# Kernel optimization log

Measured on AMD Instinct MI355X. Metric: run time of the kernel, lower is better.

Reference implementation:

```python
import jax, jax.numpy as jnp
import numpy as np

APPERTURE = 256
LN_EPS = 1e-3  # keras LayerNormalization default


def _layernorm(x, gamma, beta):
    mu = jnp.mean(x, axis=-1, keepdims=True)
    var = jnp.mean(jnp.square(x - mu), axis=-1, keepdims=True)
    return (x - mu) * jax.lax.rsqrt(var + LN_EPS) * gamma + beta


def setup_inputs() -> dict:
    key = jax.random.key(0)
    ks = jax.random.split(key, 8)
    n, d = 4096, 1024
    s = 0.02
    return {
        "x": jax.random.normal(ks[0], (1, n, d), jnp.float32),
        "wk": s * jax.random.normal(ks[1], (d, d), jnp.float32),
        "wq": s * jax.random.normal(ks[2], (d, d), jnp.float32),
        "wv": s * jax.random.normal(ks[3], (d, d), jnp.float32),
        "wo": s * jax.random.normal(ks[4], (d, d), jnp.float32),
        "wka": s * jax.random.normal(ks[5], (d, d), jnp.float32),
        "bka": jnp.zeros((d,), jnp.float32),
        "wkd": s * jax.random.normal(ks[6], (d, 1), jnp.float32),
        "bkd": jnp.zeros((1,), jnp.float32),
        "g_y": jnp.ones((d,), jnp.float32),
        "b_y": jnp.zeros((d,), jnp.float32),
        "g_ka": jnp.ones((d,), jnp.float32),
        "b_ka": jnp.zeros((d,), jnp.float32),
    }


def reference(x, wk, wq, wv, wo, wka, bka, wkd, bkd, g_y, b_y, g_ka, b_ka):
    m = x.shape[2]
    xf = x.reshape(-1, m)            # (n, m); seqlen == max_seqlen so no pad/trunc
    n = xf.shape[0]
    K = xf @ wk                      # (n, d)
    Q = (xf @ wq) * 0.06             # (n, d)
    V = xf @ wv                      # (n, d)
    logits = Q @ K.T                 # (n, n)
    # banded (apperture) mask: entries with |i-j| > apperture -> -inf
    idx = jnp.arange(n)
    band = jnp.abs(idx[:, None] - idx[None, :]) <= APPERTURE
    logits = jnp.where(band, logits, -jnp.inf)
    weights = jax.nn.softmax(logits, axis=0)   # softmax over queries (axis 0), as in original
    # y = transpose(V^T @ W) = W^T @ V
    y = weights.T @ V                # (n, d)
    y = y @ wo + xf                  # output_linear (no bias) + residual
    y = _layernorm(y, g_y, b_y)
    y = jax.nn.relu(y @ wka + bka)
    y = _layernorm(y, g_ka, b_ka)
    y = jax.nn.sigmoid(y @ wkd + bkd)  # (n, 1)
    return y.reshape(1, -1)            # (1, n)
```

## Files before the change

kernel.cpp:

```cpp
#include <hip/hip_runtime.h>
#include <hip/hip_bf16.h>
#include <math.h>

typedef __hip_bfloat16 bf16;
typedef __attribute__((ext_vector_type(8))) short bf16x8;
typedef __attribute__((ext_vector_type(4))) float f32x4;

#define NROW 4096
#define DIM  1024
#define APP  256
#define KQS  2048
#define WIN  640
#define VTPW 4608

__device__ __forceinline__ unsigned short f2bu(float f) {
    bf16 h = __float2bfloat16(f);
    return *reinterpret_cast<unsigned short*>(&h);
}
__device__ __forceinline__ float bu2f(unsigned short u) {
    bf16 h; *reinterpret_cast<unsigned short*>(&h) = u;
    return __bfloat162float(h);
}
__device__ __forceinline__ unsigned pk2(float a, float b) {
    return (unsigned)f2bu(a) | ((unsigned)f2bu(b) << 16);
}
__device__ __forceinline__ void gload_lds16(const void* g, void* l) {
    __builtin_amdgcn_global_load_lds(
        (const __attribute__((address_space(1))) unsigned int*)g,
        (__attribute__((address_space(3))) unsigned int*)l, 16, 0, 0);
}

__global__ __launch_bounds__(256) void zero_pads_kernel(bf16* __restrict__ Vtp) {
    int idx = blockIdx.x * 256 + threadIdx.x;
    int row = idx >> 7;
    int c4  = idx & 127;
    int col = (c4 < 64) ? (c4 * 4) : (4352 + (c4 - 64) * 4);
    *(uint2*)(Vtp + (size_t)row * VTPW + col) = (uint2){0u, 0u};
}

__global__ __launch_bounds__(256) void cast_x_kernel(const float* __restrict__ x,
                                                     bf16* __restrict__ xb) {
    int idx = blockIdx.x * 256 + threadIdx.x;
    float4 v = ((const float4*)x)[idx];
    uint2 o; o.x = pk2(v.x, v.y); o.y = pk2(v.z, v.w);
    ((uint2*)xb)[idx] = o;
}

struct WPtrs { const float* s[5]; bf16* d[5]; };
__global__ __launch_bounds__(256) void tcast_kernel(WPtrs p) {
    __shared__ float T[64][65];
    const float* in = p.s[blockIdx.z];
    bf16* out = p.d[blockIdx.z];
    const int t = threadIdx.x;
    const int r0 = blockIdx.x * 64, c0 = blockIdx.y * 64;
    if (blockIdx.z == 4) {
        #pragma unroll
        for (int c = 0; c < 4; ++c) {
            int row = (t >> 4) + c * 16, col = (t & 15) * 4;
            float4 v = *(const float4*)(in + (size_t)(r0 + row) * 1024 + c0 + col);
            uint2 o; o.x = pk2(v.x, v.y); o.y = pk2(v.z, v.w);
            *(uint2*)(out + (size_t)(r0 + row) * 1024 + c0 + col) = o;
        }
        return;
    }
    #pragma unroll
    for (int c = 0; c < 4; ++c) {
        int row = (t >> 4) + c * 16, col = (t & 15) * 4;
        float4 v = *(const float4*)(in + (size_t)(r0 + row) * 1024 + c0 + col);
        T[row][col] = v.x; T[row][col + 1] = v.y; T[row][col + 2] = v.z; T[row][col + 3] = v.w;
    }
    __syncthreads();
    #pragma unroll
    for (int c = 0; c < 4; ++c) {
        int orow = (t >> 4) + c * 16, ocol = (t & 15) * 4;
        uint2 o;
        o.x = pk2(T[ocol][orow], T[ocol + 1][orow]);
        o.y = pk2(T[ocol + 2][orow], T[ocol + 3][orow]);
        *(uint2*)(out + (size_t)(c0 + orow) * 1024 + r0 + ocol) = o;
    }
}

template <int BM, int BN>
__global__ __launch_bounds__(256) void gemm_bt(
    const bf16* __restrict__ A, int lda, const bf16* __restrict__ Bt, int ldb,
    bf16* __restrict__ C, int ldc, int K,
    float alpha, const float* __restrict__ bias, int relu, int pv)
{
    constexpr int WM = BM / 2, WN = BN / 2, AI = WM / 16, BJ = WN / 16;
    __shared__ bf16 As[BM * 64];
    __shared__ bf16 Bs[BN * 64];
    const int t = threadIdx.x, l = t & 63, w = t >> 6;
    const int wr = w >> 1, wc = w & 1;
    const int jl = l & 15, g = l >> 4;
    const int m0 = blockIdx.y * BM, n0 = blockIdx.x * BN;
    const bf16* Btb = pv ? (Bt + (size_t)(m0 >> 7) * 128) : Bt;

    f32x4 acc[AI][BJ];
    #pragma unroll
    for (int i = 0; i < AI; ++i)
        #pragma unroll
        for (int j = 0; j < BJ; ++j) acc[i][j] = (f32x4){0.f, 0.f, 0.f, 0.f};

    for (int kk = 0; kk < K; kk += 64) {
        __syncthreads();
        #pragma unroll
        for (int c = 0; c < BM / 32; ++c) {
            int q = t + c * 256;
            int row = q >> 3;
            int kel = ((q & 7) ^ (row & 7)) << 3;
            gload_lds16(A + (size_t)(m0 + row) * lda + kk + kel,
                        (char*)As + (c * 256 + w * 64) * 16);
        }
        #pragma unroll
        for (int c = 0; c < BN / 32; ++c) {
            int q = t + c * 256;
            int row = q >> 3;
            int kel = ((q & 7) ^ (row & 7)) << 3;
            gload_lds16(Btb + (size_t)(n0 + row) * ldb + kk + kel,
                        (char*)Bs + (c * 256 + w * 64) * 16);
        }
        __syncthreads();
        #pragma unroll
        for (int ks = 0; ks < 2; ++ks) {
            bf16x8 af[AI], bfr[BJ];
            #pragma unroll
            for (int i = 0; i < AI; ++i) {
                int ra = wr * WM + i * 16 + jl;
                af[i] = *(const bf16x8*)((char*)As + ra * 128 + ((ks * 64 + g * 16) ^ ((ra & 7) << 4)));
            }
            #pragma unroll
            for (int j = 0; j < BJ; ++j) {
                int rb = wc * WN + j * 16 + jl;
                bfr[j] = *(const bf16x8*)((char*)Bs + rb * 128 + ((ks * 64 + g * 16) ^ ((rb & 7) << 4)));
            }
            #pragma unroll
            for (int i = 0; i < AI; ++i)
                #pragma unroll
                for (int j = 0; j < BJ; ++j)
                    acc[i][j] = __builtin_amdgcn_mfma_f32_16x16x32_bf16(af[i], bfr[j], acc[i][j], 0, 0, 0);
        }
    }

    const int g4 = g * 4;
    #pragma unroll
    for (int j = 0; j < BJ; ++j) {
        int col = n0 + wc * WN + j * 16 + jl;
        float bv = bias ? bias[col] : 0.f;
        #pragma unroll
        for (int i = 0; i < AI; ++i) {
            int rowb = m0 + wr * WM + i * 16 + g4;
            #pragma unroll
            for (int r = 0; r < 4; ++r) {
                float vv = alpha * acc[i][j][r] + bv;
                if (relu) vv = fmaxf(vv, 0.f);
                C[(size_t)(rowb + r) * ldc + col] = __float2bfloat16(vv);
            }
        }
    }
}

__global__ __launch_bounds__(256) void score_gemm(const bf16* __restrict__ KQ,
                                                  bf16* __restrict__ St)
{
    constexpr int WM = 32, WN = 64, AI = 2, BJ = 4;
    __shared__ bf16 As[64 * 64];
    __shared__ bf16 Bs[128 * 64];
    const int t = threadIdx.x, l = t & 63, w = t >> 6;
    const int wr = w >> 1, wc = w & 1;
    const int jl = l & 15, g = l >> 4;
    const int tt = blockIdx.y;
    const int c0 = blockIdx.x * 64;
    const int win0 = tt * 128 - APP;
    const bf16* Qb = KQ + 1024;
    const bf16* Kb = KQ + (size_t)tt * 128 * KQS;

    f32x4 acc[AI][BJ];
    #pragma unroll
    for (int i = 0; i < AI; ++i)
        #pragma unroll
        for (int j = 0; j < BJ; ++j) acc[i][j] = (f32x4){0.f, 0.f, 0.f, 0.f};

    for (int kk = 0; kk < DIM; kk += 64) {
        __syncthreads();
        #pragma unroll
        for (int c = 0; c < 2; ++c) {
            int q = t + c * 256;
            int row = q >> 3;
            int kel = ((q & 7) ^ (row & 7)) << 3;
            int rg = win0 + c0 + row;
            rg = min(max(rg, 0), NROW - 1);
            gload_lds16(Qb + (size_t)rg * KQS + kk + kel,
                        (char*)As + (c * 256 + w * 64) * 16);
        }
        #pragma unroll
        for (int c = 0; c < 4; ++c) {
            int q = t + c * 256;
            int row = q >> 3;
            int kel = ((q & 7) ^ (row & 7)) << 3;
            gload_lds16(Kb + (size_t)row * KQS + kk + kel,
                        (char*)Bs + (c * 256 + w * 64) * 16);
        }
        __syncthreads();
        #pragma unroll
        for (int ks = 0; ks < 2; ++ks) {
            bf16x8 af[AI], bfr[BJ];
            #pragma unroll
            for (int i = 0; i < AI; ++i) {
                int ra = wr * WM + i * 16 + jl;
                af[i] = *(const bf16x8*)((char*)As + ra * 128 + ((ks * 64 + g * 16) ^ ((ra & 7) << 4)));
            }
            #pragma unroll
            for (int j = 0; j < BJ; ++j) {
                int rb = wc * WN + j * 16 + jl;
                bfr[j] = *(const bf16x8*)((char*)Bs + rb * 128 + ((ks * 64 + g * 16) ^ ((rb & 7) << 4)));
            }
            #pragma unroll
            for (int i = 0; i < AI; ++i)
                #pragma unroll
                for (int j = 0; j < BJ; ++j)
                    acc[i][j] = __builtin_amdgcn_mfma_f32_16x16x32_bf16(af[i], bfr[j], acc[i][j], 0, 0, 0);
        }
    }

    const int g4 = g * 4;
    #pragma unroll
    for (int j = 0; j < BJ; ++j) {
        int coll = wc * WN + j * 16 + jl;
        bf16* strow = St + (size_t)(tt * 128 + coll) * WIN;
        #pragma unroll
        for (int i = 0; i < AI; ++i) {
            int iwb = c0 + wr * WM + i * 16 + g4;
            #pragma unroll
            for (int r = 0; r < 4; ++r)
                strow[iwb + r] = __float2bfloat16(0.06f * acc[i][j][r]);
        }
    }
}

__global__ __launch_bounds__(256) void softmax_band(bf16* __restrict__ St)
{
    const int w = threadIdx.x >> 6, l = threadIdx.x & 63;
    const int j = blockIdx.x * 4 + w;
    const int tt = j >> 7, jt = j & 127;
    unsigned* row = (unsigned*)(St + (size_t)j * WIN);
    const int lo = max(jt, 256 - 128 * tt);
    const int hi = min(jt + 512, 4351 - 128 * tt);
    unsigned u[5]; float v[10];
    #pragma unroll
    for (int c = 0; c < 5; ++c) u[c] = row[l + 64 * c];
    float m = -3e38f;
    #pragma unroll
    for (int c = 0; c < 5; ++c) {
        int iw = 2 * (l + 64 * c);
        v[2 * c]     = (iw >= lo && iw <= hi)         ? bu2f((unsigned short)(u[c] & 0xffff)) : -3e38f;
        v[2 * c + 1] = (iw + 1 >= lo && iw + 1 <= hi) ? bu2f((unsigned short)(u[c] >> 16))    : -3e38f;
        m = fmaxf(m, fmaxf(v[2 * c], v[2 * c + 1]));
    }
    #pragma unroll
    for (int off = 32; off > 0; off >>= 1) m = fmaxf(m, __shfl_xor(m, off));
    float s = 0.f;
    #pragma unroll
    for (int c = 0; c < 10; ++c) {
        float e = (v[c] > -1e37f) ? __expf(v[c] - m) : 0.f;
        v[c] = e; s += e;
    }
    #pragma unroll
    for (int off = 32; off > 0; off >>= 1) s += __shfl_xor(s, off);
    const float inv = 1.f / s;
    #pragma unroll
    for (int c = 0; c < 5; ++c)
        row[l + 64 * c] = pk2(v[2 * c] * inv, v[2 * c + 1] * inv);
}

__global__ __launch_bounds__(256) void ln_kernel(
    const bf16* __restrict__ T, const float* __restrict__ X,
    const float* __restrict__ g, const float* __restrict__ b, bf16* __restrict__ O)
{
    __shared__ float red1[4], red2[4];
    const int r = blockIdx.x, t = threadIdx.x, lane = t & 63, w = t >> 6;
    ushort4 tv = ((const ushort4*)(T + (size_t)r * DIM))[t];
    float v0 = bu2f(tv.x), v1 = bu2f(tv.y), v2 = bu2f(tv.z), v3 = bu2f(tv.w);
    if (X) {
        float4 xv = ((const float4*)(X + (size_t)r * DIM))[t];
        v0 += xv.x; v1 += xv.y; v2 += xv.z; v3 += xv.w;
    }
    float s = v0 + v1 + v2 + v3;
    #pragma unroll
    for (int off = 32; off > 0; off >>= 1) s += __shfl_xor(s, off);
    if (lane == 0) red1[w] = s;
    __syncthreads();
    float mu = (red1[0] + red1[1] + red1[2] + red1[3]) * (1.f / DIM);
    float d0 = v0 - mu, d1 = v1 - mu, d2 = v2 - mu, d3 = v3 - mu;
    float s2 = d0 * d0 + d1 * d1 + d2 * d2 + d3 * d3;
    #pragma unroll
    for (int off = 32; off > 0; off >>= 1) s2 += __shfl_xor(s2, off);
    if (lane == 0) red2[w] = s2;
    __syncthreads();
    float var = (red2[0] + red2[1] + red2[2] + red2[3]) * (1.f / DIM);
    float rstd = rsqrtf(var + 1e-3f);
    float4 gv = ((const float4*)g)[t];
    float4 bv = ((const float4*)b)[t];
    uint2 o;
    o.x = pk2(d0 * rstd * gv.x + bv.x, d1 * rstd * gv.y + bv.y);
    o.y = pk2(d2 * rstd * gv.z + bv.z, d3 * rstd * gv.w + bv.w);
    ((uint2*)(O + (size_t)r * DIM))[t] = o;
}

__global__ __launch_bounds__(256) void final_kernel(
    const bf16* __restrict__ Y, const float* __restrict__ wkd,
    const float* __restrict__ bkd, float* __restrict__ out)
{
    const int lane = threadIdx.x & 63, w = threadIdx.x >> 6;
    const int r = blockIdx.x * 4 + w;
    const bf16* yr = Y + (size_t)r * DIM;
    float s = 0.f;
    #pragma unroll
    for (int c = 0; c < 4; ++c) {
        ushort4 yv = ((const ushort4*)yr)[lane * 4 + c];
        float4 wv = ((const float4*)wkd)[lane * 4 + c];
        s += bu2f(yv.x) * wv.x + bu2f(yv.y) * wv.y + bu2f(yv.z) * wv.z + bu2f(yv.w) * wv.w;
    }
    #pragma unroll
    for (int off = 32; off > 0; off >>= 1) s += __shfl_xor(s, off);
    if (lane == 0) out[r] = 1.f / (1.f + __expf(-(s + bkd[0])));
}

extern "C" void kernel_launch(void* const* d_in, const int* in_sizes, int n_in,
                              void* d_out, int out_size, void* d_ws, size_t ws_size,
                              hipStream_t stream) {
    const float* x    = (const float*)d_in[0];
    const float* wk   = (const float*)d_in[1];
    const float* wq   = (const float*)d_in[2];
    const float* wv   = (const float*)d_in[3];
    const float* wo   = (const float*)d_in[4];
    const float* wka  = (const float*)d_in[5];
    const float* bka  = (const float*)d_in[6];
    const float* wkd  = (const float*)d_in[7];
    const float* bkd  = (const float*)d_in[8];
    const float* g_y  = (const float*)d_in[9];
    const float* b_y  = (const float*)d_in[10];
    const float* g_ka = (const float*)d_in[11];
    const float* b_ka = (const float*)d_in[12];
    float* out = (float*)d_out;

    char* ws = (char*)d_ws;
    const size_t MB = 1u << 20;
    const size_t NM = (size_t)NROW * DIM;
    bf16* woT  = (bf16*)(ws);
    bf16* wkaT = (bf16*)(ws + 2 * MB);
    bf16* fKQ  = (bf16*)(ws + 4 * MB);
    bf16* Vtp  = (bf16*)(ws + 20 * MB);
    bf16* St   = (bf16*)(ws + 30 * MB);
    bf16* fT   = (bf16*)(ws + 36 * MB);
    bf16* wkT  = (bf16*)(ws + 36 * MB);
    bf16* wqT  = (bf16*)(ws + 38 * MB);
    bf16* wvB  = (bf16*)(ws + 40 * MB);
    bf16* wvoT = (bf16*)(ws + 42 * MB);
    bf16* xb   = (bf16*)(ws + 44 * MB);
    bf16* fL1  = fKQ + NM;
    bf16* fRel = Vtp;
    bf16* fT2  = fT;

    zero_pads_kernel<<<512, 256, 0, stream>>>(Vtp);
    cast_x_kernel<<<NROW * DIM / 4 / 256, 256, 0, stream>>>(x, xb);
    WPtrs wp;
    wp.s[0] = wk;  wp.s[1] = wq;  wp.s[2] = wo;  wp.s[3] = wka;  wp.s[4] = wv;
    wp.d[0] = wkT; wp.d[1] = wqT; wp.d[2] = woT; wp.d[3] = wkaT; wp.d[4] = wvB;
    tcast_kernel<<<dim3(16, 16, 5), 256, 0, stream>>>(wp);

    gemm_bt<64, 64><<<dim3(16, 16), 256, 0, stream>>>(
        woT, DIM, wvB, DIM, wvoT, DIM, DIM, 1.f, nullptr, 0, 0);
    gemm_bt<128, 128><<<dim3(16, 32), 256, 0, stream>>>(
        xb, DIM, wkT, DIM, fKQ, KQS, DIM, 1.f, nullptr, 0, 0);
    gemm_bt<64, 128><<<dim3(32, 16), 256, 0, stream>>>(
        wvoT, DIM, xb, DIM, Vtp + 256, VTPW, DIM, 1.f, nullptr, 0, 0);

    score_gemm<<<dim3(WIN / 64, NROW / 128), 256, 0, stream>>>(fKQ, St);
    softmax_band<<<NROW / 4, 256, 0, stream>>>(St);
    gemm_bt<64, 128><<<dim3(8, 64), 256, 0, stream>>>(
        St, WIN, Vtp, VTPW, fT, DIM, WIN, 1.f, nullptr, 0, 1);

    ln_kernel<<<NROW, 256, 0, stream>>>(fT, x, g_y, b_y, fL1);
    gemm_bt<128, 64><<<dim3(16, 32), 256, 0, stream>>>(
        fL1, DIM, wkaT, DIM, fRel, DIM, DIM, 1.f, bka, 1, 0);
    ln_kernel<<<NROW, 256, 0, stream>>>(fRel, nullptr, g_ka, b_ka, fT2);
    final_kernel<<<NROW / 4, 256, 0, stream>>>(fT2, wkd, bkd, out);
}
```

Baseline: 141.7 us.

## Fold Wq·Wk^T into a combined weight and fuse final layernorm with sigmoid head

Precomputes Wq·Wk^T as one weight product alongside Wo·Wv in a batched mini-GEMM. A single n×d projection of x then replaces the previous n×2d K/Q projection, and score_gemm uses raw bf16 x as the key side. The second layernorm is fused with the wkd dot product and sigmoid into one kernel, which removes an intermediate buffer write and read. The combined-weight path adds one extra bf16 rounding step, and the transpose/cast kernel's role assignment and the workspace layout are reshuffled to match.

New measurement: 130.5 us. 7.9% less time.

```diff
diff --git a/kernel.cpp b/kernel.cpp
--- a/kernel.cpp
+++ b/kernel.cpp
@@ -9,7 +9,6 @@
 #define NROW 4096
 #define DIM  1024
 #define APP  256
-#define KQS  2048
 #define WIN  640
 #define VTPW 4608
 
@@ -53,7 +52,7 @@
     bf16* out = p.d[blockIdx.z];
     const int t = threadIdx.x;
     const int r0 = blockIdx.x * 64, c0 = blockIdx.y * 64;
-    if (blockIdx.z == 4) {
+    if (blockIdx.z < 3) {
         #pragma unroll
         for (int c = 0; c < 4; ++c) {
             int row = (t >> 4) + c * 16, col = (t & 15) * 4;
@@ -159,7 +158,75 @@
     }
 }
 
-__global__ __launch_bounds__(256) void score_gemm(const bf16* __restrict__ KQ,
+struct MiniPtrs { const bf16* A[2]; const bf16* Bt[2]; bf16* C[2]; };
+__global__ __launch_bounds__(256) void gemm_mini(MiniPtrs p) {
+    constexpr int BM = 64, BN = 64, WM = 32, WN = 32, AI = 2, BJ = 2;
+    __shared__ bf16 As[BM * 64];
+    __shared__ bf16 Bs[BN * 64];
+    const bf16* A  = p.A[blockIdx.z];
+    const bf16* Bt = p.Bt[blockIdx.z];
+    bf16* C        = p.C[blockIdx.z];
+    const int t = threadIdx.x, l = t & 63, w = t >> 6;
+    const int wr = w >> 1, wc = w & 1;
+    const int jl = l & 15, g = l >> 4;
+    const int m0 = blockIdx.y * BM, n0 = blockIdx.x * BN;
+
+    f32x4 acc[AI][BJ];
+    #pragma unroll
+    for (int i = 0; i < AI; ++i)
+        #pragma unroll
+        for (int j = 0; j < BJ; ++j) acc[i][j] = (f32x4){0.f, 0.f, 0.f, 0.f};
+
+    for (int kk = 0; kk < DIM; kk += 64) {
+        __syncthreads();
+        #pragma unroll
+        for (int c = 0; c < 2; ++c) {
+            int q = t + c * 256;
+            int row = q >> 3;
+            int kel = ((q & 7) ^ (row & 7)) << 3;
+            gload_lds16(A + (size_t)(m0 + row) * DIM + kk + kel,
+                        (char*)As + (c * 256 + w * 64) * 16);
+            gload_lds16(Bt + (size_t)(n0 + row) * DIM + kk + kel,
+                        (char*)Bs + (c * 256 + w * 64) * 16);
+        }
+        __syncthreads();
+        #pragma unroll
+        for (int ks = 0; ks < 2; ++ks) {
+            bf16x8 af[AI], bfr[BJ];
+            #pragma unroll
+            for (int i = 0; i < AI; ++i) {
+                int ra = wr * WM + i * 16 + jl;
+                af[i] = *(const bf16x8*)((char*)As + ra * 128 + ((ks * 64 + g * 16) ^ ((ra & 7) << 4)));
+            }
+            #pragma unroll
+            for (int j = 0; j < BJ; ++j) {
+                int rb = wc * WN + j * 16 + jl;
+                bfr[j] = *(const bf16x8*)((char*)Bs + rb * 128 + ((ks * 64 + g * 16) ^ ((rb & 7) << 4)));
+            }
+            #pragma unroll
+            for (int i = 0; i < AI; ++i)
+                #pragma unroll
+                for (int j = 0; j < BJ; ++j)
+                    acc[i][j] = __builtin_amdgcn_mfma_f32_16x16x32_bf16(af[i], bfr[j], acc[i][j], 0, 0, 0);
+        }
+    }
+
+    const int g4 = g * 4;
+    #pragma unroll
+    for (int j = 0; j < BJ; ++j) {
+        int col = n0 + wc * WN + j * 16 + jl;
+        #pragma unroll
+        for (int i = 0; i < AI; ++i) {
+            int rowb = m0 + wr * WM + i * 16 + g4;
+            #pragma unroll
+            for (int r = 0; r < 4; ++r)
+                C[(size_t)(rowb + r) * DIM + col] = __float2bfloat16(acc[i][j][r]);
+        }
+    }
+}
+
+__global__ __launch_bounds__(256) void score_gemm(const bf16* __restrict__ Qh,
+                                                  const bf16* __restrict__ xb,
                                                   bf16* __restrict__ St)
 {
     constexpr int WM = 32, WN = 64, AI = 2, BJ = 4;
@@ -171,8 +238,7 @@
     const int tt = blockIdx.y;
     const int c0 = blockIdx.x * 64;
     const int win0 = tt * 128 - APP;
-    const bf16* Qb = KQ + 1024;
-    const bf16* Kb = KQ + (size_t)tt * 128 * KQS;
+    const bf16* Kb = xb + (size_t)tt * 128 * DIM;
 
     f32x4 acc[AI][BJ];
     #pragma unroll
@@ -189,7 +255,7 @@
             int kel = ((q & 7) ^ (row & 7)) << 3;
             int rg = win0 + c0 + row;
             rg = min(max(rg, 0), NROW - 1);
-            gload_lds16(Qb + (size_t)rg * KQS + kk + kel,
+            gload_lds16(Qh + (size_t)rg * DIM + kk + kel,
                         (char*)As + (c * 256 + w * 64) * 16);
         }
         #pragma unroll
@@ -197,7 +263,7 @@
             int q = t + c * 256;
             int row = q >> 3;
             int kel = ((q & 7) ^ (row & 7)) << 3;
-            gload_lds16(Kb + (size_t)row * KQS + kk + kel,
+            gload_lds16(Kb + (size_t)row * DIM + kk + kel,
                         (char*)Bs + (c * 256 + w * 64) * 16);
         }
         __syncthreads();
@@ -306,23 +372,41 @@
     ((uint2*)(O + (size_t)r * DIM))[t] = o;
 }
 
-__global__ __launch_bounds__(256) void final_kernel(
-    const bf16* __restrict__ Y, const float* __restrict__ wkd,
-    const float* __restrict__ bkd, float* __restrict__ out)
+__global__ __launch_bounds__(256) void lnfinal_kernel(
+    const bf16* __restrict__ T, const float* __restrict__ g, const float* __restrict__ b,
+    const float* __restrict__ wkd, const float* __restrict__ bkd, float* __restrict__ out)
 {
-    const int lane = threadIdx.x & 63, w = threadIdx.x >> 6;
-    const int r = blockIdx.x * 4 + w;
-    const bf16* yr = Y + (size_t)r * DIM;
-    float s = 0.f;
-    #pragma unroll
-    for (int c = 0; c < 4; ++c) {
-        ushort4 yv = ((const ushort4*)yr)[lane * 4 + c];
-        float4 wv = ((const float4*)wkd)[lane * 4 + c];
-        s += bu2f(yv.x) * wv.x + bu2f(yv.y) * wv.y + bu2f(yv.z) * wv.z + bu2f(yv.w) * wv.w;
-    }
+    __shared__ float red1[4], red2[4], red3[4];
+    const int r = blockIdx.x, t = threadIdx.x, lane = t & 63, w = t >> 6;
+    ushort4 tv = ((const ushort4*)(T + (size_t)r * DIM))[t];
+    float v0 = bu2f(tv.x), v1 = bu2f(tv.y), v2 = bu2f(tv.z), v3 = bu2f(tv.w);
+    float s = v0 + v1 + v2 + v3;
     #pragma unroll
     for (int off = 32; off > 0; off >>= 1) s += __shfl_xor(s, off);
-    if (lane == 0) out[r] = 1.f / (1.f + __expf(-(s + bkd[0])));
+    if (lane == 0) red1[w] = s;
+    __syncthreads();
+    float mu = (red1[0] + red1[1] + red1[2] + red1[3]) * (1.f / DIM);
+    float d0 = v0 - mu, d1 = v1 - mu, d2 = v2 - mu, d3 = v3 - mu;
+    float s2 = d0 * d0 + d1 * d1 + d2 * d2 + d3 * d3;
+    #pragma unroll
+    for (int off = 32; off > 0; off >>= 1) s2 += __shfl_xor(s2, off);
+    if (lane == 0) red2[w] = s2;
+    __syncthreads();
+    float var = (red2[0] + red2[1] + red2[2] + red2[3]) * (1.f / DIM);
+    float rstd = rsqrtf(var + 1e-3f);
+    float4 gv = ((const float4*)g)[t];
+    float4 bv = ((const float4*)b)[t];
+    float4 wv = ((const float4*)wkd)[t];
+    float s3 = (d0 * rstd * gv.x + bv.x) * wv.x + (d1 * rstd * gv.y + bv.y) * wv.y
+             + (d2 * rstd * gv.z + bv.z) * wv.z + (d3 * rstd * gv.w + bv.w) * wv.w;
+    #pragma unroll
+    for (int off = 32; off > 0; off >>= 1) s3 += __shfl_xor(s3, off);
+    if (lane == 0) red3[w] = s3;
+    __syncthreads();
+    if (t == 0) {
+        float tot = red3[0] + red3[1] + red3[2] + red3[3];
+        out[r] = 1.f / (1.f + __expf(-(tot + bkd[0])));
+    }
 }
 
 extern "C" void kernel_launch(void* const* d_in, const int* in_sizes, int n_in,
@@ -345,37 +429,39 @@
 
     char* ws = (char*)d_ws;
     const size_t MB = 1u << 20;
-    const size_t NM = (size_t)NROW * DIM;
-    bf16* woT  = (bf16*)(ws);
-    bf16* wkaT = (bf16*)(ws + 2 * MB);
-    bf16* fKQ  = (bf16*)(ws + 4 * MB);
-    bf16* Vtp  = (bf16*)(ws + 20 * MB);
-    bf16* St   = (bf16*)(ws + 30 * MB);
-    bf16* fT   = (bf16*)(ws + 36 * MB);
-    bf16* wkT  = (bf16*)(ws + 36 * MB);
-    bf16* wqT  = (bf16*)(ws + 38 * MB);
-    bf16* wvB  = (bf16*)(ws + 40 * MB);
-    bf16* wvoT = (bf16*)(ws + 42 * MB);
-    bf16* xb   = (bf16*)(ws + 44 * MB);
-    bf16* fL1  = fKQ + NM;
-    bf16* fRel = Vtp;
-    bf16* fT2  = fT;
+    bf16* wkB  = (bf16*)(ws);
+    bf16* wqB  = (bf16*)(ws + 2 * MB);
+    bf16* wvB  = (bf16*)(ws + 4 * MB);
+    bf16* woT  = (bf16*)(ws + 6 * MB);
+    bf16* wkaT = (bf16*)(ws + 8 * MB);
+    bf16* WqkT = (bf16*)(ws + 10 * MB);
+    bf16* wvoT = (bf16*)(ws + 12 * MB);
+    bf16* xb   = (bf16*)(ws + 14 * MB);
+    bf16* Qh   = (bf16*)(ws + 22 * MB);
+    bf16* Vtp  = (bf16*)(ws + 30 * MB);
+    bf16* St   = (bf16*)(ws + 40 * MB);
+    bf16* fT   = (bf16*)(ws + 46 * MB);
+    bf16* fL1  = (bf16*)(ws + 54 * MB);
+    bf16* fRel = (bf16*)(ws + 62 * MB);
 
     zero_pads_kernel<<<512, 256, 0, stream>>>(Vtp);
     cast_x_kernel<<<NROW * DIM / 4 / 256, 256, 0, stream>>>(x, xb);
     WPtrs wp;
-    wp.s[0] = wk;  wp.s[1] = wq;  wp.s[2] = wo;  wp.s[3] = wka;  wp.s[4] = wv;
-    wp.d[0] = wkT; wp.d[1] = wqT; wp.d[2] = woT; wp.d[3] = wkaT; wp.d[4] = wvB;
+    wp.s[0] = wk;  wp.s[1] = wq;  wp.s[2] = wv;  wp.s[3] = wo;  wp.s[4] = wka;
+    wp.d[0] = wkB; wp.d[1] = wqB; wp.d[2] = wvB; wp.d[3] = woT; wp.d[4] = wkaT;
     tcast_kernel<<<dim3(16, 16, 5), 256, 0, stream>>>(wp);
 
-    gemm_bt<64, 64><<<dim3(16, 16), 256, 0, stream>>>(
-        woT, DIM, wvB, DIM, wvoT, DIM, DIM, 1.f, nullptr, 0, 0);
-    gemm_bt<128, 128><<<dim3(16, 32), 256, 0, stream>>>(
-        xb, DIM, wkT, DIM, fKQ, KQS, DIM, 1.f, nullptr, 0, 0);
+    MiniPtrs mp;
+    mp.A[0] = wkB; mp.Bt[0] = wqB; mp.C[0] = WqkT;
+    mp.A[1] = woT; mp.Bt[1] = wvB; mp.C[1] = wvoT;
+    gemm_mini<<<dim3(16, 16, 2), 256, 0, stream>>>(mp);
+
+    gemm_bt<128, 64><<<dim3(16, 32), 256, 0, stream>>>(
+        xb, DIM, WqkT, DIM, Qh, DIM, DIM, 1.f, nullptr, 0, 0);
     gemm_bt<64, 128><<<dim3(32, 16), 256, 0, stream>>>(
         wvoT, DIM, xb, DIM, Vtp + 256, VTPW, DIM, 1.f, nullptr, 0, 0);
 
-    score_gemm<<<dim3(WIN / 64, NROW / 128), 256, 0, stream>>>(fKQ, St);
+    score_gemm<<<dim3(WIN / 64, NROW / 128), 256, 0, stream>>>(Qh, xb, St);
     softmax_band<<<NROW / 4, 256, 0, stream>>>(St);
     gemm_bt<64, 128><<<dim3(8, 64), 256, 0, stream>>>(
         St, WIN, Vtp, VTPW, fT, DIM, WIN, 1.f, nullptr, 0, 1);
@@ -383,6 +469,5 @@
     ln_kernel<<<NROW, 256, 0, stream>>>(fT, x, g_y, b_y, fL1);
     gemm_bt<128, 64><<<dim3(16, 32), 256, 0, stream>>>(
         fL1, DIM, wkaT, DIM, fRel, DIM, DIM, 1.f, bka, 1, 0);
-    ln_kernel<<<NROW, 256, 0, stream>>>(fRel, nullptr, g_ka, b_ka, fT2);
-    final_kernel<<<NROW / 4, 256, 0, stream>>>(fT2, wkd, bkd, out);
-}
+    lnfinal_kernel<<<NROW, 256, 0, stream>>>(fRel, g_ka, b_ka, wkd, bkd, out);
+}
```
